# Kernel tuning notes

Hardware: AMD Instinct MI355X
Metric: run time of the kernel (lower is better)

## Reference

```python
import jax, jax.numpy as jnp
import numpy as np

H = 8          # num_heads
FOCUS = 3      # focusing_factor
EPS = 1e-6


def _disagreement(h):
    # h: [B, Hn, N, d]; mean of pairwise cosine-sim matrix with diagonal zeroed
    B, Hn, N, d = h.shape
    hn = h / jnp.maximum(jnp.linalg.norm(h, axis=-1, keepdims=True), 1e-12)
    sim_sum = jnp.sum(jnp.einsum('bhnd,bhmd->bhnm', hn, hn))
    diag_sum = jnp.sum(hn * hn)  # diagonal entries of the sim matrix
    return (sim_sum - diag_sum) / (B * Hn * N * N)


def setup_inputs() -> dict:
    key = jax.random.key(0)
    ks = jax.random.split(key, 10)
    B, N, C, K = 4, 1024, 512, 10
    s = 0.02
    return {
        'Q': jax.random.normal(ks[0], (B, N, C), jnp.float32),
        'adj_mat': jax.random.randint(ks[1], (B, N, K), 0, N),
        'Wq': jax.random.normal(ks[2], (C, C), jnp.float32) * s,
        'bq': jnp.zeros((C,), jnp.float32),
        'Wk': jax.random.normal(ks[3], (C, C), jnp.float32) * s,
        'bk': jnp.zeros((C,), jnp.float32),
        'Wv': jax.random.normal(ks[4], (C, C), jnp.float32) * s,
        'bv': jnp.zeros((C,), jnp.float32),
        'scale_p': jnp.zeros((1, 1, C), jnp.float32),  # torch init: zeros
        'Wconv': jax.random.normal(ks[5], (C, C, K + 1), jnp.float32) * s,
        'bconv': jnp.zeros((C,), jnp.float32),
        'W2': jax.random.normal(ks[6], (C, C), jnp.float32) * s,
        'b2': jnp.zeros((C,), jnp.float32),
        'ln_g': jnp.ones((C,), jnp.float32),
        'ln_b': jnp.zeros((C,), jnp.float32),
        'Wo': jax.random.normal(ks[7], (C, C), jnp.float32) * s,
        'bo': jnp.zeros((C,), jnp.float32),
    }


def _forward(Q, adj_mat, Wq, bq, Wk, bk, Wv, bv, scale_p, Wconv, bconv,
             W2, b2, ln_g, ln_b, Wo, bo):
    B, N, C = Q.shape
    d = C // H
    q = Q @ Wq + bq
    k = Q @ Wk + bk
    v = Q @ Wv + bv

    # LocalFeatureExtractor on v: gather K neighbors, conv over (channel, K+1) window
    neigh = v[jnp.arange(B)[:, None, None], adj_mat]          # [B,N,K,C]
    feats = jnp.concatenate([v[:, :, None, :], neigh], axis=2)  # [B,N,K+1,C]
    conv = jnp.einsum('bntc,oct->bno', feats, Wconv) + bconv   # full-window conv1d
    x_local = conv @ W2 + b2                                   # [B,N,C]

    # kernelized q/k with softplus scale and focused normalization
    q = jax.nn.relu(q) + EPS
    k = jax.nn.relu(k) + EPS
    scale = jax.nn.softplus(scale_p)
    q = q / scale
    k = k / scale

    def focus(x):
        n = jnp.linalg.norm(x, axis=-1, keepdims=True)
        return (x / (n + EPS)) ** FOCUS * n

    q = focus(q)
    k = focus(k)

    q = q.reshape(B, N, H, d).transpose(0, 2, 1, 3)
    k = k.reshape(B, N, H, d).transpose(0, 2, 1, 3)
    vh = v.reshape(B, N, H, d).transpose(0, 2, 1, 3)

    # linear attention: z normalization and kv summarization
    z = 1.0 / (jnp.einsum('bhnd,bhd->bhn', q, k.mean(axis=2)) + EPS)  # [B,H,N]
    kv = jnp.einsum('bhnd,bhne->bhde', k, vh) / N                     # [B,H,d,d]
    x = jnp.einsum('bhnd,bhde->bhne', q, kv) * z[..., None]           # [B,H,N,d]

    loss_local = _disagreement(vh)
    loss_kv = _disagreement(kv)

    x = x.transpose(0, 2, 1, 3).reshape(B, N, C) + x_local
    x4 = x.reshape(B, H, N, d)  # raw memory reinterpretation, matches torch .reshape
    loss_out = _disagreement(x4)
    loss = (loss_local + loss_out + loss_kv) / 3.0
    x = x4.reshape(B, N, C)

    # out_proj: LayerNorm then Linear
    mu = x.mean(axis=-1, keepdims=True)
    var = jnp.mean((x - mu) ** 2, axis=-1, keepdims=True)
    xn = (x - mu) / jnp.sqrt(var + 1e-5) * ln_g + ln_b
    out = xn @ Wo + bo
    return out, loss


def reference(Q, adj_mat, Wq, bq, Wk, bk, Wv, bv, scale_p, Wconv, bconv,
              W2, b2, ln_g, ln_b, Wo, bo):
    return _forward(Q, adj_mat, Wq, bq, Wk, bk, Wv, bv, scale_p, Wconv, bconv,
                    W2, b2, ln_g, ln_b, Wo, bo)
```

## Files before the change

kernel.cpp:

```cpp
#include <hip/hip_runtime.h>
#include <math.h>

#define TOK_TOTAL 4096
#define KNB 10
#define MATE 2097152

typedef __attribute__((ext_vector_type(8))) short short8;
typedef __attribute__((ext_vector_type(4))) float floatx4;
typedef unsigned short ushort;

__device__ __forceinline__ floatx4 mfma16(short8 a, short8 b, floatx4 c) {
  return __builtin_amdgcn_mfma_f32_16x16x32_bf16(a, b, c, 0, 0, 0);
}

__device__ __forceinline__ ushort f2bf(float f) {
  union { float f; unsigned int u; } x; x.f = f;
  unsigned int r = x.u + 0x7fffu + ((x.u >> 16) & 1u);
  return (ushort)(r >> 16);
}

__device__ __forceinline__ float bf2f(ushort u) {
  union { unsigned int u; float f; } x; x.u = ((unsigned int)u) << 16;
  return x.f;
}

__device__ __forceinline__ float lane_bcast(float v, int l) {
  union { float f; int i; } x; x.f = v;
  x.i = __builtin_amdgcn_readlane(x.i, l);
  return x.f;
}

__device__ __forceinline__ void glds16(const ushort* g, ushort* l) {
  __builtin_amdgcn_global_load_lds((const __attribute__((address_space(1))) void*)g,
                                   (__attribute__((address_space(3))) void*)l, 16, 0, 0);
}

__device__ __forceinline__ float wave_reduce_sum(float v) {
#pragma unroll
  for (int m = 32; m >= 1; m >>= 1) v += __shfl_xor(v, m, 64);
  return v;
}

__device__ __forceinline__ float block_reduce_sum_256(float v, float* red) {
  v = wave_reduce_sum(v);
  __syncthreads();
  if ((threadIdx.x & 63) == 0) red[threadIdx.x >> 6] = v;
  __syncthreads();
  return red[0] + red[1] + red[2] + red[3];
}

__global__ __launch_bounds__(256) void prep_kernel(const float* __restrict__ Wq,
                                                   const float* __restrict__ Wk,
                                                   const float* __restrict__ Wv,
                                                   const float* __restrict__ W2p,
                                                   const float* __restrict__ Wo,
                                                   const float* __restrict__ Wconv,
                                                   const float* __restrict__ Q,
                                                   const float* __restrict__ bq,
                                                   const float* __restrict__ bk,
                                                   const float* __restrict__ bv,
                                                   ushort* __restrict__ WT,
                                                   ushort* __restrict__ BcY,
                                                   float* __restrict__ biasqkv,
                                                   ushort* __restrict__ Qb) {
  int blk = blockIdx.x;
  if (blk < 1280) {
    __shared__ float tile[32][33];
    int zz = blk >> 8, rem = blk & 255;
    const float* W = (zz == 0) ? Wq : (zz == 1) ? Wk : (zz == 2) ? Wv
                     : (zz == 3) ? W2p : Wo;
    ushort* Wt = WT + (size_t)zz * 262144;
    int n0 = (rem & 15) * 32, k0 = (rem >> 4) * 32;
    int tx = threadIdx.x & 31, ty = threadIdx.x >> 5;
#pragma unroll
    for (int i = 0; i < 32; i += 8)
      tile[ty + i][tx] = W[(size_t)(k0 + ty + i) * 512 + n0 + tx];
    __syncthreads();
#pragma unroll
    for (int i = 0; i < 32; i += 8)
      Wt[(size_t)(n0 + ty + i) * 512 + k0 + tx] = f2bf(tile[tx][ty + i]);
  } else if (blk < 2304) {
    int i = (blk - 1280) * 256 + threadIdx.x;
    const float* src = Wconv + (size_t)i * 11;
    int o = i >> 9, c = i & 511;
#pragma unroll
    for (int t = 0; t < 11; ++t)
      BcY[(((size_t)(t * 512 + o)) << 9) + c] = f2bf(src[t]);
  } else if (blk == 2304) {
    for (int i = threadIdx.x; i < 1536; i += 256)
      biasqkv[i] = (i < 512) ? bq[i] : ((i < 1024) ? bk[i - 512] : bv[i - 1024]);
  } else {
    int i = (blk - 2305) * 256 + threadIdx.x;
    float4 v = *(const float4*)(Q + (size_t)i * 4);
    Qb[(size_t)i * 4 + 0] = f2bf(v.x);
    Qb[(size_t)i * 4 + 1] = f2bf(v.y);
    Qb[(size_t)i * 4 + 2] = f2bf(v.z);
    Qb[(size_t)i * 4 + 3] = f2bf(v.w);
  }
}

__global__ __launch_bounds__(256, 3) void gemm128(const ushort* __restrict__ A,
                                                  const ushort* __restrict__ Bt,
                                                  ushort* __restrict__ Cb,
                                                  int Ktot, int Ncols) {
  __shared__ __align__(16) ushort As[3][4096];
  __shared__ __align__(16) ushort Bs[3][4096];
  int tid = threadIdx.x, w = tid >> 6, lane = tid & 63;
  int lm = lane & 15, kq = lane >> 4;
  int row0 = blockIdx.y * 128, col0 = blockIdx.x * 128;
  int wm = w >> 1, wn = w & 1;

  bool isA = (w < 2);
  const ushort* gs[4];
  int go[4];
#pragma unroll
  for (int i = 0; i < 4; ++i) {
    int slab = (w & 1) * 4 + i;
    const ushort* base = isA ? (A + (size_t)(row0 + slab * 16 + lm) * Ktot)
                             : (Bt + (size_t)(col0 + slab * 16 + lm) * Ktot);
    gs[i] = base + kq * 8;
    go[i] = slab * 512;
  }

  floatx4 acc[4][4];
#pragma unroll
  for (int i = 0; i < 4; ++i)
#pragma unroll
    for (int j = 0; j < 4; ++j)
#pragma unroll
      for (int e = 0; e < 4; ++e) acc[i][j][e] = 0.f;

#pragma unroll
  for (int i = 0; i < 4; ++i) glds16(gs[i], (isA ? As[0] : Bs[0]) + go[i]);
#pragma unroll
  for (int i = 0; i < 4; ++i) glds16(gs[i] + 32, (isA ? As[1] : Bs[1]) + go[i]);
  asm volatile("s_waitcnt vmcnt(4)" ::: "memory");
  __builtin_amdgcn_s_barrier();

  int nsteps = Ktot >> 5;
  for (int s = 0; s < nsteps; ++s) {
    int cur = s % 3;
    if (s + 2 < nsteps) {
      int nb = (s + 2) % 3;
      ushort* dst = (isA ? As[nb] : Bs[nb]);
      int koff = (s + 2) << 5;
#pragma unroll
      for (int i = 0; i < 4; ++i) glds16(gs[i] + koff, dst + go[i]);
    }
    const ushort* Acur = As[cur];
    const ushort* Bcur = Bs[cur];
    short8 a[4], b[4];
#pragma unroll
    for (int mt = 0; mt < 4; ++mt)
      a[mt] = *(const short8*)(&Acur[(wm * 4 + mt) * 512 + lane * 8]);
#pragma unroll
    for (int nt = 0; nt < 4; ++nt)
      b[nt] = *(const short8*)(&Bcur[(wn * 4 + nt) * 512 + lane * 8]);
#pragma unroll
    for (int mt = 0; mt < 4; ++mt)
#pragma unroll
      for (int nt = 0; nt < 4; ++nt)
        acc[mt][nt] = mfma16(a[mt], b[nt], acc[mt][nt]);
    if (s + 1 < nsteps) {
      if (s + 2 < nsteps) {
        asm volatile("s_waitcnt vmcnt(4)" ::: "memory");
      } else {
        asm volatile("s_waitcnt vmcnt(0)" ::: "memory");
      }
      __builtin_amdgcn_s_barrier();
    }
  }

#pragma unroll
  for (int mt = 0; mt < 4; ++mt) {
#pragma unroll
    for (int nt = 0; nt < 4; ++nt) {
      int col = col0 + wn * 64 + nt * 16 + lm;
#pragma unroll
      for (int r = 0; r < 4; ++r) {
        int row = row0 + wm * 64 + mt * 16 + kq * 4 + r;
        Cb[(size_t)row * Ncols + col] = f2bf(acc[mt][nt][r]);
      }
    }
  }
}

__global__ __launch_bounds__(256, 4) void gemm128_qkv(const ushort* __restrict__ A,
                                                      const ushort* __restrict__ Bt,
                                                      const float* __restrict__ bias,
                                                      float* __restrict__ outf,
                                                      ushort* __restrict__ vb) {
  __shared__ __align__(16) ushort As[2][4096];
  __shared__ __align__(16) ushort Bs[2][4096];
  int tid = threadIdx.x, w = tid >> 6, lane = tid & 63;
  int lm = lane & 15, kq = lane >> 4;
  int row0 = blockIdx.y * 128, col0 = blockIdx.x * 128;
  int wm = w >> 1, wn = w & 1;

  bool isA = (w < 2);
  const ushort* gs[4];
  int go[4];
#pragma unroll
  for (int i = 0; i < 4; ++i) {
    int slab = (w & 1) * 4 + i;
    const ushort* base = isA ? (A + (size_t)(row0 + slab * 16 + lm) * 512)
                             : (Bt + (size_t)(col0 + slab * 16 + lm) * 512);
    gs[i] = base + kq * 8;
    go[i] = slab * 512;
  }

  floatx4 acc[4][4];
#pragma unroll
  for (int i = 0; i < 4; ++i)
#pragma unroll
    for (int j = 0; j < 4; ++j)
#pragma unroll
      for (int e = 0; e < 4; ++e) acc[i][j][e] = 0.f;

#pragma unroll
  for (int i = 0; i < 4; ++i)
    glds16(gs[i], (isA ? As[0] : Bs[0]) + go[i]);

  for (int s = 0; s < 16; ++s) {
    int buf = s & 1;
    __syncthreads();
    if (s + 1 < 16) {
      int koff = (s + 1) << 5;
      ushort* dst = (isA ? As[buf ^ 1] : Bs[buf ^ 1]);
#pragma unroll
      for (int i = 0; i < 4; ++i) glds16(gs[i] + koff, dst + go[i]);
    }
    short8 a[4], b[4];
#pragma unroll
    for (int mt = 0; mt < 4; ++mt)
      a[mt] = *(const short8*)(&As[buf][(wm * 4 + mt) * 512 + lane * 8]);
#pragma unroll
    for (int nt = 0; nt < 4; ++nt)
      b[nt] = *(const short8*)(&Bs[buf][(wn * 4 + nt) * 512 + lane * 8]);
#pragma unroll
    for (int mt = 0; mt < 4; ++mt)
#pragma unroll
      for (int nt = 0; nt < 4; ++nt)
        acc[mt][nt] = mfma16(a[mt], b[nt], acc[mt][nt]);
  }

#pragma unroll
  for (int mt = 0; mt < 4; ++mt) {
#pragma unroll
    for (int nt = 0; nt < 4; ++nt) {
      int col = col0 + wn * 64 + nt * 16 + lm;
      int mat = col >> 9, cc = col & 511;
      float bs = bias[col];
#pragma unroll
      for (int r = 0; r < 4; ++r) {
        int row = row0 + wm * 64 + mt * 16 + kq * 4 + r;
        float val = acc[mt][nt][r] + bs;
        size_t idx = (size_t)row * 512 + cc;
        outf[(size_t)mat * MATE + idx] = val;
        if (mat == 2) vb[idx] = f2bf(val);
      }
    }
  }
}

__global__ __launch_bounds__(256) void gather_add_bias(const ushort* __restrict__ Y,
                                                       const int* __restrict__ adj,
                                                       const float* __restrict__ bias,
                                                       ushort* __restrict__ convb) {
  int n = (blockIdx.x << 1) + (threadIdx.x >> 7);
  int b10 = (n >> 10) << 10;
  int o = (threadIdx.x & 127) << 2;
  float4 bs = *(const float4*)(bias + o);
  float a0 = bs.x, a1 = bs.y, a2 = bs.z, a3 = bs.w;
#pragma unroll
  for (int t = 0; t < 11; ++t) {
    int src = (t == 0) ? n : (b10 + adj[(size_t)n * KNB + (t - 1)]);
    const ushort* p = Y + (size_t)src * 5632 + (size_t)t * 512 + o;
    uint2 u = *(const uint2*)p;
    a0 += bf2f((ushort)(u.x & 0xffff));
    a1 += bf2f((ushort)(u.x >> 16));
    a2 += bf2f((ushort)(u.y & 0xffff));
    a3 += bf2f((ushort)(u.y >> 16));
  }
  uint2 w;
  w.x = (unsigned)f2bf(a0) | ((unsigned)f2bf(a1) << 16);
  w.y = (unsigned)f2bf(a2) | ((unsigned)f2bf(a3) << 16);
  *(uint2*)(convb + (size_t)n * 512 + o) = w;
}

__global__ __launch_bounds__(256) void gather_add(const ushort* __restrict__ Y,
                                                  const int* __restrict__ adj,
                                                  float* __restrict__ convf,
                                                  int t0, int ntaps, int ncols) {
  int n = blockIdx.x;
  int b10 = (n >> 10) << 10;
  int o = threadIdx.x * 2;
  float a0 = 0.f, a1 = 0.f;
  for (int t = t0; t < t0 + ntaps; ++t) {
    int src = (t == 0) ? n : (b10 + adj[(size_t)n * KNB + (t - 1)]);
    const ushort* p = Y + (size_t)src * ncols + (size_t)(t - t0) * 512 + o;
    a0 += bf2f(p[0]);
    a1 += bf2f(p[1]);
  }
  convf[(size_t)n * 512 + o] += a0;
  convf[(size_t)n * 512 + o + 1] += a1;
}

__global__ __launch_bounds__(256) void convbias_cast(const float* __restrict__ cf,
                                                     const float* __restrict__ bias,
                                                     ushort* __restrict__ cb) {
  int i = blockIdx.x * 256 + threadIdx.x;
  float4 v = *(const float4*)(cf + (size_t)i * 4);
  int c = (i * 4) & 511;
  cb[(size_t)i * 4 + 0] = f2bf(v.x + bias[c + 0]);
  cb[(size_t)i * 4 + 1] = f2bf(v.y + bias[c + 1]);
  cb[(size_t)i * 4 + 2] = f2bf(v.z + bias[c + 2]);
  cb[(size_t)i * 4 + 3] = f2bf(v.w + bias[c + 3]);
}

__global__ __launch_bounds__(256) void gemm64(const ushort* __restrict__ A,
                                              const ushort* __restrict__ Bt,
                                              const float* __restrict__ bias,
                                              float* __restrict__ Cf,
                                              ushort* __restrict__ Cb,
                                              int Ktot) {
  __shared__ __align__(16) ushort As[2][4096];
  __shared__ __align__(16) ushort Bs[2][4096];
  int tid = threadIdx.x, w = tid >> 6, lane = tid & 63;
  int lm = lane & 15, kq = lane >> 4;
  int row0 = blockIdx.y * 64, col0 = blockIdx.x * 64;
  int wm = w >> 1, wn = w & 1;

  const ushort* gsrc[4];
  int goff[4];
  bool isA = (w < 2);
#pragma unroll
  for (int i = 0; i < 4; ++i) {
    int l = w * 4 + i, t, j;
    const ushort* base;
    if (l < 8) { t = l >> 1; j = l & 1; base = A + (size_t)(row0 + t * 16 + lm) * Ktot; }
    else { int lb = l - 8; t = lb >> 1; j = lb & 1; base = Bt + (size_t)(col0 + t * 16 + lm) * Ktot; }
    gsrc[i] = base + j * 32 + kq * 8;
    goff[i] = t * 1024 + j * 512;
  }

  floatx4 acc[2][2];
#pragma unroll
  for (int i = 0; i < 2; ++i)
#pragma unroll
    for (int j = 0; j < 2; ++j)
#pragma unroll
      for (int e = 0; e < 4; ++e) acc[i][j][e] = 0.f;

#pragma unroll
  for (int i = 0; i < 4; ++i)
    glds16(gsrc[i], (isA ? As[0] : Bs[0]) + goff[i]);

  int nsteps = Ktot >> 6;
  for (int s = 0; s < nsteps; ++s) {
    int buf = s & 1;
    __syncthreads();
    if (s + 1 < nsteps) {
      int koff = (s + 1) << 6;
      ushort* dst = (isA ? As[buf ^ 1] : Bs[buf ^ 1]);
#pragma unroll
      for (int i = 0; i < 4; ++i) glds16(gsrc[i] + koff, dst + goff[i]);
    }
#pragma unroll
    for (int j = 0; j < 2; ++j) {
      short8 a0 = *(const short8*)(&As[buf][(wm * 2 + 0) * 1024 + j * 512 + lane * 8]);
      short8 a1 = *(const short8*)(&As[buf][(wm * 2 + 1) * 1024 + j * 512 + lane * 8]);
      short8 b0 = *(const short8*)(&Bs[buf][(wn * 2 + 0) * 1024 + j * 512 + lane * 8]);
      short8 b1 = *(const short8*)(&Bs[buf][(wn * 2 + 1) * 1024 + j * 512 + lane * 8]);
      acc[0][0] = mfma16(a0, b0, acc[0][0]);
      acc[0][1] = mfma16(a0, b1, acc[0][1]);
      acc[1][0] = mfma16(a1, b0, acc[1][0]);
      acc[1][1] = mfma16(a1, b1, acc[1][1]);
    }
  }

  int colb = col0 + wn * 32;
  int rowb = row0 + wm * 32 + kq * 4;
#pragma unroll
  for (int mt = 0; mt < 2; ++mt) {
#pragma unroll
    for (int nt = 0; nt < 2; ++nt) {
      int col = colb + nt * 16 + lm;
      float bs = bias[col];
#pragma unroll
      for (int r = 0; r < 4; ++r) {
        int row = rowb + mt * 16 + r;
        float val = acc[mt][nt][r] + bs;
        size_t idx = (size_t)row * 512 + col;
        if (Cf) Cf[idx] = val;
        if (Cb) Cb[idx] = f2bf(val);
      }
    }
  }
}

__global__ __launch_bounds__(256) void focus_kernel(float* __restrict__ x,
                                                    const float* __restrict__ scale_p) {
  __shared__ float red[4];
  int row = blockIdx.x;
  float* p = x + (size_t)row * 512;
  int tid = threadIdx.x;
  float sp0 = scale_p[tid], sp1 = scale_p[tid + 256];
  float sc0 = sp0 > 20.f ? sp0 : log1pf(expf(sp0));
  float sc1 = sp1 > 20.f ? sp1 : log1pf(expf(sp1));
  float v0 = (fmaxf(p[tid], 0.f) + 1e-6f) / sc0;
  float v1 = (fmaxf(p[tid + 256], 0.f) + 1e-6f) / sc1;
  float tot = block_reduce_sum_256(v0 * v0 + v1 * v1, red);
  float n = sqrtf(tot);
  float np = n + 1e-6f;
  float f = n / (np * np * np);
  p[tid] = v0 * v0 * v0 * f;
  p[tid + 256] = v1 * v1 * v1 * f;
}

__global__ __launch_bounds__(256) void kv_kernel(const float* __restrict__ kf,
                                                 const float* __restrict__ v,
                                                 float* __restrict__ kv,
                                                 float* __restrict__ Sacc,
                                                 float* __restrict__ Dacc,
                                                 float* __restrict__ kmean) {
  __shared__ float Ks[16][64];
  __shared__ float Vs[16][64];
  __shared__ float Spart[64];
  __shared__ float Kpart[64];
  __shared__ float Dpart;
  int bh = blockIdx.x >> 3, chunk = blockIdx.x & 7;
  int b = bh >> 3, h = bh & 7;
  int tid = threadIdx.x;
  int lr = tid >> 4, lc = (tid & 15) << 2;
  int tx = tid & 15, ty = tid >> 4;
  if (tid < 64) { Spart[tid] = 0.f; Kpart[tid] = 0.f; }
  if (tid == 0) Dpart = 0.f;
  __syncthreads();
  const float* kbase = kf + (size_t)b * 524288 + h * 64 + (size_t)chunk * 128 * 512;
  const float* vbase = v + (size_t)b * 524288 + h * 64 + (size_t)chunk * 128 * 512;
  float acc[4][4] = {};
  float Sloc[4] = {0.f, 0.f, 0.f, 0.f};
  float Kloc[4] = {0.f, 0.f, 0.f, 0.f};
  float Dloc = 0.f;
  for (int n0 = 0; n0 < 128; n0 += 16) {
    float4 ke = *(const float4*)(kbase + (size_t)(n0 + lr) * 512 + lc);
    *(float4*)(&Ks[lr][lc]) = ke;
    Kloc[0] += ke.x; Kloc[1] += ke.y; Kloc[2] += ke.z; Kloc[3] += ke.w;
    float4 ve = *(const float4*)(vbase + (size_t)(n0 + lr) * 512 + lc);
    *(float4*)(&Vs[lr][lc]) = ve;
    __syncthreads();
    float sq = ve.x * ve.x + ve.y * ve.y + ve.z * ve.z + ve.w * ve.w;
#pragma unroll
    for (int m = 1; m < 16; m <<= 1) sq += __shfl_xor(sq, m, 64);
    float cn = fmaxf(sqrtf(sq), 1e-12f);
    Sloc[0] += ve.x / cn; Sloc[1] += ve.y / cn;
    Sloc[2] += ve.z / cn; Sloc[3] += ve.w / cn;
    if ((tid & 15) == 0) Dloc += sq / (cn * cn);
#pragma unroll
    for (int kk = 0; kk < 16; ++kk) {
      float a[4], bb[4];
#pragma unroll
      for (int i = 0; i < 4; ++i) a[i] = Ks[kk][ty * 4 + i];
#pragma unroll
      for (int j = 0; j < 4; ++j) bb[j] = Vs[kk][tx * 4 + j];
#pragma unroll
      for (int i = 0; i < 4; ++i)
#pragma unroll
        for (int j = 0; j < 4; ++j) acc[i][j] += a[i] * bb[j];
    }
    __syncthreads();
  }
#pragma unroll
  for (int i = 0; i < 4; ++i)
#pragma unroll
    for (int j = 0; j < 4; ++j)
      atomicAdd(&kv[(size_t)bh * 4096 + (ty * 4 + i) * 64 + tx * 4 + j],
                acc[i][j] * (1.f / 1024.f));
#pragma unroll
  for (int i = 0; i < 4; ++i) {
    atomicAdd(&Spart[lc + i], Sloc[i]);
    atomicAdd(&Kpart[lc + i], Kloc[i]);
  }
  if ((tid & 15) == 0) atomicAdd(&Dpart, Dloc);
  __syncthreads();
  if (tid < 64) {
    atomicAdd(&Sacc[bh * 64 + tid], Spart[tid]);
    atomicAdd(&kmean[b * 512 + h * 64 + tid], Kpart[tid] * (1.f / 1024.f));
  }
  if (tid == 64) atomicAdd(&Dacc[bh], Dpart);
}

__global__ __launch_bounds__(512, 4) void attn_ln_kernel(const float* __restrict__ qf,
                                                         const float* __restrict__ kvf,
                                                         const float* __restrict__ kmean,
                                                         const float* __restrict__ x_local,
                                                         const float* __restrict__ g,
                                                         const float* __restrict__ bp,
                                                         ushort* __restrict__ xn,
                                                         float* __restrict__ Sacc,
                                                         float* __restrict__ Dacc,
                                                         float* __restrict__ Skv,
                                                         float* __restrict__ Dkv) {
  __shared__ __align__(16) ushort kvs[32768];
  __shared__ float red[16];
  __shared__ float Sl[8][64];
  __shared__ float Dl[8];
  int r0 = blockIdx.x << 3;
  int b = r0 >> 10;
  int c = threadIdx.x, wv = c >> 6, lane = c & 63;
  const float4* kvg = (const float4*)(kvf + (size_t)b * 32768);
#pragma unroll
  for (int i = 0; i < 16; ++i) {
    float4 kvv = kvg[c + i * 512];
    int o = (c + i * 512) << 2;
    kvs[o + 0] = f2bf(kvv.x); kvs[o + 1] = f2bf(kvv.y);
    kvs[o + 2] = f2bf(kvv.z); kvs[o + 3] = f2bf(kvv.w);
  }
  float kmr = kmean[b * 512 + c];
  float gr = g[c], bpr = bp[c];
  __syncthreads();
  unsigned int kvr[32];
#pragma unroll
  for (int i = 0; i < 32; ++i) {
    unsigned int lo = kvs[wv * 4096 + (2 * i) * 64 + lane];
    unsigned int hi = kvs[wv * 4096 + (2 * i + 1) * 64 + lane];
    kvr[i] = lo | (hi << 16);
  }
  float Sreg = 0.f, Dreg = 0.f;
  for (int r = 0; r < 8; ++r) {
    int row = r0 + r;
    float qv = qf[(size_t)row * 512 + c];
    float xl = x_local[(size_t)row * 512 + c];
    float zd = wave_reduce_sum(qv * kmr);
    float zz = 1.f / (zd + 1e-6f);
    float s = 0.f;
#pragma unroll
    for (int i = 0; i < 32; ++i) {
      union { unsigned int u; float f; } lo, hi;
      lo.u = kvr[i] << 16;
      hi.u = kvr[i] & 0xffff0000u;
      s += lane_bcast(qv, 2 * i) * lo.f;
      s += lane_bcast(qv, 2 * i + 1) * hi.f;
    }
    float xv = s * zz + xl;
    float s1 = wave_reduce_sum(xv);
    float s2 = wave_reduce_sum(xv * xv);
    if (lane == 0) { red[wv] = s1; red[8 + wv] = s2; }
    __syncthreads();
    float tsum = red[0] + red[1] + red[2] + red[3] + red[4] + red[5] + red[6] + red[7];
    float tsq = red[8] + red[9] + red[10] + red[11] + red[12] + red[13] + red[14] + red[15];
    __syncthreads();
    float mu = tsum * (1.f / 512.f);
    float var = tsq * (1.f / 512.f) - mu * mu;
    float inv = rsqrtf(fmaxf(var, 0.f) + 1e-5f);
    xn[(size_t)row * 512 + c] = f2bf((xv - mu) * inv * gr + bpr);
    float norm = fmaxf(sqrtf(s2), 1e-12f);
    Sreg += xv / norm;
    Dreg += s2 / (norm * norm);
  }
  Sl[wv][lane] = Sreg;
  if (lane == 0) Dl[wv] = Dreg;
  __syncthreads();
  int gx = b * 8 + ((r0 & 1023) >> 7);
  if (c < 64) {
    float ssum = 0.f;
#pragma unroll
    for (int ww = 0; ww < 8; ++ww) ssum += Sl[ww][c];
    atomicAdd(&Sacc[gx * 64 + c], ssum);
  } else if (c == 64) {
    float dsum = 0.f;
#pragma unroll
    for (int ww = 0; ww < 8; ++ww) dsum += Dl[ww];
    atomicAdd(&Dacc[gx], dsum);
  }
  if ((blockIdx.x & 127) == 0) {
    float S2 = 0.f, D2 = 0.f;
#pragma unroll
    for (int i = 0; i < 32; ++i) {
      union { unsigned int u; float f; } lo, hi;
      lo.u = kvr[i] << 16;
      hi.u = kvr[i] & 0xffff0000u;
      float sq = wave_reduce_sum(lo.f * lo.f);
      float nrm = fmaxf(sqrtf(sq), 1e-12f);
      float hn = lo.f / nrm;
      S2 += hn; D2 += hn * hn;
      sq = wave_reduce_sum(hi.f * hi.f);
      nrm = fmaxf(sqrtf(sq), 1e-12f);
      hn = hi.f / nrm;
      S2 += hn; D2 += hn * hn;
    }
    float dt = wave_reduce_sum(D2);
    atomicAdd(&Skv[(b * 8 + wv) * 64 + lane], S2);
    if (lane == 0) atomicAdd(&Dkv[b * 8 + wv], dt);
  }
}

__global__ __launch_bounds__(64) void disagree_final_all(const float* __restrict__ Sall,
                                                         const float* __restrict__ Dall,
                                                         float s0, float s1, float s2,
                                                         float* __restrict__ loss) {
  int set = blockIdx.x >> 5, gg = blockIdx.x & 31;
  int l = threadIdx.x;
  float sv = Sall[set * 2048 + gg * 64 + l];
  float sim = wave_reduce_sum(sv * sv);
  if (l == 0) {
    float scale = (set == 0) ? s0 : (set == 1) ? s1 : s2;
    atomicAdd(loss, (sim - Dall[set * 32 + gg]) * scale);
  }
}

extern "C" void kernel_launch(void* const* d_in, const int* in_sizes, int n_in,
                              void* d_out, int out_size, void* d_ws, size_t ws_size,
                              hipStream_t stream) {
  const float* Q       = (const float*)d_in[0];
  const int*   adj     = (const int*)d_in[1];
  const float* Wq      = (const float*)d_in[2];
  const float* bq      = (const float*)d_in[3];
  const float* Wk      = (const float*)d_in[4];
  const float* bk      = (const float*)d_in[5];
  const float* Wv      = (const float*)d_in[6];
  const float* bv      = (const float*)d_in[7];
  const float* scale_p = (const float*)d_in[8];
  const float* Wconv   = (const float*)d_in[9];
  const float* bconv   = (const float*)d_in[10];
  const float* W2      = (const float*)d_in[11];
  const float* b2      = (const float*)d_in[12];
  const float* ln_g    = (const float*)d_in[13];
  const float* ln_b    = (const float*)d_in[14];
  const float* Wo      = (const float*)d_in[15];
  const float* bo      = (const float*)d_in[16];

  float* out = (float*)d_out;
  float* loss_slot = out + MATE;

  float* ws = (float*)d_ws;
  float* q0      = ws;
  float* k0      = q0 + MATE;
  float* v       = k0 + MATE;
  float* x_local = v + MATE;
  float* convf   = x_local + MATE;
  ushort* Qb    = (ushort*)(convf + MATE);
  ushort* vb    = Qb + MATE;
  ushort* convb = vb + MATE;
  ushort* xnb   = convb + MATE;
  ushort* WqT   = xnb + MATE;
  ushort* W2T   = WqT + 3 * 262144;
  ushort* WoT   = W2T + 262144;
  ushort* BcY   = WoT + 262144;
  float* biasqkv = (float*)(BcY + 5632 * 512);
  float* kmean = biasqkv + 1536;
  float* kvbuf = kmean + 2048;
  float* Sv    = kvbuf + 131072;
  float* Skv   = Sv + 2048;
  float* Sx    = Skv + 2048;
  float* Dv    = Sx + 2048;
  float* Dkv   = Dv + 32;
  float* Dx    = Dkv + 32;
  float* ytail = Dx + 32;
  ushort* Ybf  = (ushort*)ytail;

  size_t used_floats = (size_t)(ytail - ws);
  size_t avail_floats = (ws_size / 4 > used_floats) ? (ws_size / 4 - used_floats) : 0;
  int TC = (int)(avail_floats / (MATE / 2));
  if (TC < 1) TC = 1;
  if (TC > 11) TC = 11;

  hipMemsetAsync(loss_slot, 0, sizeof(float), stream);
  hipMemsetAsync(kmean, 0, (2048 + 131072 + 3 * 2048 + 96) * sizeof(float), stream);

  prep_kernel<<<4353, 256, 0, stream>>>(Wq, Wk, Wv, W2, Wo, Wconv, Q,
                                        bq, bk, bv, WqT, BcY, biasqkv, Qb);

  gemm128_qkv<<<dim3(12, 32), 256, 0, stream>>>(Qb, WqT, biasqkv, q0, vb);

  if (TC >= 11) {
    gemm128<<<dim3(44, 32), 256, 0, stream>>>(vb, BcY, Ybf, 512, 5632);
    gather_add_bias<<<2048, 256, 0, stream>>>(Ybf, adj, bconv, convb);
  } else {
    hipMemsetAsync(convf, 0, MATE * sizeof(float), stream);
    for (int t0 = 0; t0 < 11; t0 += TC) {
      int nt = (11 - t0 < TC) ? (11 - t0) : TC;
      int ncols = nt * 512;
      gemm128<<<dim3(ncols / 128, 32), 256, 0, stream>>>(
          vb, BcY + (size_t)(t0 * 512) * 512, Ybf, 512, ncols);
      gather_add<<<4096, 256, 0, stream>>>(Ybf, adj, convf, t0, nt, ncols);
    }
    convbias_cast<<<2048, 256, 0, stream>>>(convf, bconv, convb);
  }

  gemm64<<<dim3(8, 64), 256, 0, stream>>>(convb, W2T, b2, x_local, nullptr, 512);

  focus_kernel<<<2 * TOK_TOTAL, 256, 0, stream>>>(q0, scale_p);

  kv_kernel<<<256, 256, 0, stream>>>(k0, v, kvbuf, Sv, Dv, kmean);

  attn_ln_kernel<<<512, 512, 0, stream>>>(q0, kvbuf, kmean, x_local,
                                          ln_g, ln_b, xnb, Sx, Dx, Skv, Dkv);

  disagree_final_all<<<96, 64, 0, stream>>>(Sv, Dv,
                                            1.f / (33554432.f * 3.f),
                                            1.f / (131072.f * 3.f),
                                            1.f / (33554432.f * 3.f), loss_slot);

  gemm64<<<dim3(8, 64), 256, 0, stream>>>(xnb, WoT, bo, out, nullptr, 512);
}
```

Baseline: 292.6 us.

## Fuse q focusing into attention kernel and fold memsets into prep kernel

The q-side focused normalization (relu, softplus scale, cube and norm rescale) is now computed inside the attention/LayerNorm kernel instead of a separate focus pass, so focus_kernel only processes k and launches half as many blocks. The two memset calls are replaced by extra blocks in the prep kernel that zero the accumulator region and the loss slot. This removes a full read/write pass over q and two launches. In exchange it adds a block-wide reduction with two extra barriers per row in the attention kernel.

After: 288.1 us. About the same (-1.6%).

```diff
diff --git a/kernel.cpp b/kernel.cpp
--- a/kernel.cpp
+++ b/kernel.cpp
@@ -62,7 +62,9 @@
                                                    ushort* __restrict__ WT,
                                                    ushort* __restrict__ BcY,
                                                    float* __restrict__ biasqkv,
-                                                   ushort* __restrict__ Qb) {
+                                                   ushort* __restrict__ Qb,
+                                                   float* __restrict__ zbase,
+                                                   float* __restrict__ loss) {
   int blk = blockIdx.x;
   if (blk < 1280) {
     __shared__ float tile[32][33];
@@ -89,13 +91,20 @@
   } else if (blk == 2304) {
     for (int i = threadIdx.x; i < 1536; i += 256)
       biasqkv[i] = (i < 512) ? bq[i] : ((i < 1024) ? bk[i - 512] : bv[i - 1024]);
-  } else {
+  } else if (blk < 4353) {
     int i = (blk - 2305) * 256 + threadIdx.x;
     float4 v = *(const float4*)(Q + (size_t)i * 4);
     Qb[(size_t)i * 4 + 0] = f2bf(v.x);
     Qb[(size_t)i * 4 + 1] = f2bf(v.y);
     Qb[(size_t)i * 4 + 2] = f2bf(v.z);
     Qb[(size_t)i * 4 + 3] = f2bf(v.w);
+  } else {
+    int i = (blk - 4353) * 256 + threadIdx.x;
+    if (i < 34840) {
+      float4 z; z.x = 0.f; z.y = 0.f; z.z = 0.f; z.w = 0.f;
+      ((float4*)zbase)[i] = z;
+    }
+    if (blk == 4353 && threadIdx.x == 0) loss[0] = 0.f;
   }
 }
 
@@ -495,6 +504,7 @@
                                                          const float* __restrict__ kvf,
                                                          const float* __restrict__ kmean,
                                                          const float* __restrict__ x_local,
+                                                         const float* __restrict__ scale_p,
                                                          const float* __restrict__ g,
                                                          const float* __restrict__ bp,
                                                          ushort* __restrict__ xn,
@@ -519,6 +529,9 @@
   }
   float kmr = kmean[b * 512 + c];
   float gr = g[c], bpr = bp[c];
+  float sp = scale_p[c];
+  float sc = sp > 20.f ? sp : log1pf(expf(sp));
+  float scinv = 1.f / sc;
   __syncthreads();
   unsigned int kvr[32];
 #pragma unroll
@@ -530,8 +543,17 @@
   float Sreg = 0.f, Dreg = 0.f;
   for (int r = 0; r < 8; ++r) {
     int row = r0 + r;
-    float qv = qf[(size_t)row * 512 + c];
+    float qraw = qf[(size_t)row * 512 + c];
     float xl = x_local[(size_t)row * 512 + c];
+    float v0 = (fmaxf(qraw, 0.f) + 1e-6f) * scinv;
+    float l2 = wave_reduce_sum(v0 * v0);
+    if (lane == 0) red[wv] = l2;
+    __syncthreads();
+    float nq2 = red[0] + red[1] + red[2] + red[3] + red[4] + red[5] + red[6] + red[7];
+    __syncthreads();
+    float nq = sqrtf(nq2);
+    float npq = nq + 1e-6f;
+    float qv = v0 * v0 * v0 * (nq / (npq * npq * npq));
     float zd = wave_reduce_sum(qv * kmr);
     float zz = 1.f / (zd + 1e-6f);
     float s = 0.f;
@@ -666,11 +688,9 @@
   if (TC < 1) TC = 1;
   if (TC > 11) TC = 11;
 
-  hipMemsetAsync(loss_slot, 0, sizeof(float), stream);
-  hipMemsetAsync(kmean, 0, (2048 + 131072 + 3 * 2048 + 96) * sizeof(float), stream);
-
-  prep_kernel<<<4353, 256, 0, stream>>>(Wq, Wk, Wv, W2, Wo, Wconv, Q,
-                                        bq, bk, bv, WqT, BcY, biasqkv, Qb);
+  prep_kernel<<<4490, 256, 0, stream>>>(Wq, Wk, Wv, W2, Wo, Wconv, Q,
+                                        bq, bk, bv, WqT, BcY, biasqkv, Qb,
+                                        kmean, loss_slot);
 
   gemm128_qkv<<<dim3(12, 32), 256, 0, stream>>>(Qb, WqT, biasqkv, q0, vb);
 
@@ -691,11 +711,11 @@
 
   gemm64<<<dim3(8, 64), 256, 0, stream>>>(convb, W2T, b2, x_local, nullptr, 512);
 
-  focus_kernel<<<2 * TOK_TOTAL, 256, 0, stream>>>(q0, scale_p);
+  focus_kernel<<<TOK_TOTAL, 256, 0, stream>>>(k0, scale_p);
 
   kv_kernel<<<256, 256, 0, stream>>>(k0, v, kvbuf, Sv, Dv, kmean);
 
-  attn_ln_kernel<<<512, 512, 0, stream>>>(q0, kvbuf, kmean, x_local,
+  attn_ln_kernel<<<512, 512, 0, stream>>>(q0, kvbuf, kmean, x_local, scale_p,
                                           ln_g, ln_b, xnb, Sx, Dx, Skv, Dkv);
 
   disagree_final_all<<<96, 64, 0, stream>>>(Sv, Dv,
```
